# Performance work log

Measured on AMD Instinct MI355X. Metric: run time of the kernel, lower is better.

Reference implementation:

```python
import jax, jax.numpy as jnp
import numpy as np

NUM_HEADS = 8

def _mha(x, in_w, in_b, out_w, out_b):
    # x: [B, L, E]; in_w: [3E, E]; out_w: [E, E]
    B, L, E = x.shape
    H = NUM_HEADS
    Dh = E // H
    qkv = x @ in_w.T + in_b                      # [B, L, 3E]
    q, k, v = jnp.split(qkv, 3, axis=-1)
    # [B, H, L, Dh]
    q = q.reshape(B, L, H, Dh).transpose(0, 2, 1, 3)
    k = k.reshape(B, L, H, Dh).transpose(0, 2, 1, 3)
    v = v.reshape(B, L, H, Dh).transpose(0, 2, 1, 3)
    scale = 1.0 / jnp.sqrt(jnp.asarray(Dh, dtype=x.dtype))
    scores = jnp.einsum('bhld,bhsd->bhls', q, k) * scale   # [B, H, L, S]
    attn = jax.nn.softmax(scores, axis=-1)
    ctx = jnp.einsum('bhls,bhsd->bhld', attn, v)           # [B, H, L, Dh]
    ctx = ctx.transpose(0, 2, 1, 3).reshape(B, L, E)
    out = ctx @ out_w.T + out_b                             # [B, L, E]
    # PyTorch default average_attn_weights=True: mean over heads -> [B, L, S]
    weights = attn.mean(axis=1)
    return out, weights

def setup_inputs() -> dict:
    key = jax.random.key(0)
    ks = jax.random.split(key, 5)
    B, L, E = 4, 2048, 1024
    s = 0.02
    return {
        'hidden_states': jax.random.normal(ks[0], (B, L, E), dtype=jnp.float32),
        'in_proj_w': jax.random.normal(ks[1], (3 * E, E), dtype=jnp.float32) * s,
        'in_proj_b': jnp.zeros((3 * E,), dtype=jnp.float32),
        'out_proj_w': jax.random.normal(ks[2], (E, E), dtype=jnp.float32) * s,
        'out_proj_b': jnp.zeros((E,), dtype=jnp.float32),
        'dep_proj_w': jax.random.normal(ks[3], (E, E), dtype=jnp.float32) * s,
        'dep_proj_b': jnp.zeros((E,), dtype=jnp.float32),
    }

def reference(hidden_states, in_proj_w, in_proj_b, out_proj_w, out_proj_b, dep_proj_w, dep_proj_b):
    enhanced, attn_weights = _mha(hidden_states, in_proj_w, in_proj_b, out_proj_w, out_proj_b)
    # dependency_scores: mean over query dim then key dim -> [B]
    dependency_scores = attn_weights.mean(axis=1).mean(axis=-1)
    enhanced = enhanced @ dep_proj_w.T + dep_proj_b
    return dependency_scores, enhanced
```

## Files before the change

kernel.cpp:

```cpp
#include <hip/hip_runtime.h>


typedef __attribute__((ext_vector_type(8))) short short8;
typedef __attribute__((ext_vector_type(4))) float float4v;
typedef __attribute__((ext_vector_type(4))) int int4v;
typedef __attribute__((ext_vector_type(2))) unsigned uint2v;

__device__ inline ushort f2bf(float f) {
  union { float f; unsigned u; } v; v.f = f;
  unsigned u = v.u;
  return (ushort)((u + 0x7FFFu + ((u >> 16) & 1u)) >> 16);
}
__device__ inline float bf2f(ushort h) {
  union { unsigned u; float f; } v; v.u = ((unsigned)h) << 16;
  return v.f;
}
__device__ inline unsigned cvtpk(float lo, float hi) {
  unsigned r;
  asm("v_cvt_pk_bf16_f32 %0, %1, %2" : "=v"(r) : "v"(lo), "v"(hi));
  return r;
}

__global__ __launch_bounds__(256)
void cvt_all(const float* __restrict__ X, const float* __restrict__ Wi,
             const float* __restrict__ Wd,
             ushort* __restrict__ Xb, ushort* __restrict__ Wib,
             ushort* __restrict__ Wdb) {
  size_t i = ((size_t)blockIdx.x * 256 + threadIdx.x) * 8;
  const float* src; ushort* dst;
  if (i < 8388608)        { src = X  + i;              dst = Xb  + i; }
  else if (i < 11534336)  { src = Wi + (i - 8388608);  dst = Wib + (i - 8388608); }
  else                    { src = Wd + (i - 11534336); dst = Wdb + (i - 11534336); }
  float4v a = *(const float4v*)(src);
  float4v b = *(const float4v*)(src + 4);
  ushort o[8];
  o[0] = f2bf(a.x); o[1] = f2bf(a.y); o[2] = f2bf(a.z); o[3] = f2bf(a.w);
  o[4] = f2bf(b.x); o[5] = f2bf(b.y); o[6] = f2bf(b.z); o[7] = f2bf(b.w);
  *(int4v*)dst = *(const int4v*)o;
}

__global__ __launch_bounds__(256)
void cvtT(const float* __restrict__ Wo, ushort* __restrict__ WoT) {
  __shared__ ushort Ts[64 * 72];
  const int t = threadIdx.x;
  const int ct = blockIdx.x * 64, rt = blockIdx.y * 64;
#pragma unroll
  for (int i = 0; i < 4; i++) {
    const int row = i * 16 + (t >> 4), col4 = (t & 15) * 4;
    float4v v = *(const float4v*)(Wo + (size_t)(rt + row) * 1024 + ct + col4);
    ushort o[4] = {f2bf(v.x), f2bf(v.y), f2bf(v.z), f2bf(v.w)};
    *(uint2v*)(Ts + row * 72 + col4) = *(const uint2v*)o;
  }
  __syncthreads();
#pragma unroll
  for (int it = 0; it < 2; it++) {
    const int c = it * 256 + t;
    const int oc = c >> 3, r8 = (c & 7) * 8;
    ushort o[8];
#pragma unroll
    for (int j = 0; j < 8; j++) o[j] = Ts[(r8 + j) * 72 + oc];
    *(int4v*)(WoT + (size_t)(ct + oc) * 1024 + rt + r8) = *(const int4v*)o;
  }
}

__global__ __launch_bounds__(64)
void bck(const float* __restrict__ Wd, const float* __restrict__ bo,
         const float* __restrict__ bd, float* __restrict__ bc,
         float* __restrict__ dep) {
  const int row = blockIdx.x, lane = threadIdx.x;
  float s = 0.f;
#pragma unroll
  for (int i = 0; i < 4; i++) {
    const int j = i * 256 + lane * 4;
    float4v w = *(const float4v*)(Wd + (size_t)row * 1024 + j);
    float4v b = *(const float4v*)(bo + j);
    s += w.x * b.x + w.y * b.y + w.z * b.z + w.w * b.w;
  }
#pragma unroll
  for (int off = 1; off <= 32; off <<= 1) s += __shfl_xor(s, off);
  if (lane == 0) bc[row] = s + bd[row];
  if (row < 4 && lane == 1) dep[row] = 1.0f / 2048.0f;
}

template <bool OUT_BF16>
__global__ __launch_bounds__(256, 2)
void gemm_bt(const ushort* __restrict__ A, const ushort* __restrict__ W,
             const float* __restrict__ bias, void* __restrict__ Cv,
             int M, int N, int K) {
  __shared__ ushort As[128 * 32];
  __shared__ ushort Bs[128 * 32];
  const int t = threadIdx.x;
  const int w = t >> 6;
  const int lane = t & 63;
  const int m16 = lane & 15, quad = lane >> 4;
  const int bx = blockIdx.x, by = blockIdx.y;
  const int warpRow = w >> 1, warpCol = w & 1;

  const int srow = t >> 2;
  const int scol = (t & 3) * 8;
  const ushort* Aptr = A + (size_t)(by * 128) * K;
  const ushort* Wptr = W + (size_t)(bx * 128) * K;

  float4v zero4 = {0.f, 0.f, 0.f, 0.f};
  float4v acc[4][4];
#pragma unroll
  for (int i = 0; i < 4; i++)
#pragma unroll
    for (int j = 0; j < 4; j++) acc[i][j] = zero4;

  for (int k0 = 0; k0 < K; k0 += 32) {
    __syncthreads();
#pragma unroll
    for (int r = 0; r < 2; r++) {
      const ushort* g = Aptr + (size_t)(r * 64 + srow) * K + (k0 + scol);
      __builtin_amdgcn_global_load_lds(
          (const __attribute__((address_space(1))) void*)g,
          (__attribute__((address_space(3))) void*)(As + r * 2048 + t * 8),
          16, 0, 0);
    }
#pragma unroll
    for (int r = 0; r < 2; r++) {
      const ushort* g = Wptr + (size_t)(r * 64 + srow) * K + (k0 + scol);
      __builtin_amdgcn_global_load_lds(
          (const __attribute__((address_space(1))) void*)g,
          (__attribute__((address_space(3))) void*)(Bs + r * 2048 + t * 8),
          16, 0, 0);
    }
    __syncthreads();

    short8 af[4], bf[4];
#pragma unroll
    for (int i = 0; i < 4; i++) {
      af[i] = *(const short8*)(As + (warpRow * 64 + i * 16 + m16) * 32 + quad * 8);
      bf[i] = *(const short8*)(Bs + (warpCol * 64 + i * 16 + m16) * 32 + quad * 8);
    }
#pragma unroll
    for (int i = 0; i < 4; i++)
#pragma unroll
      for (int j = 0; j < 4; j++)
        acc[i][j] = __builtin_amdgcn_mfma_f32_16x16x32_bf16(af[i], bf[j],
                                                            acc[i][j], 0, 0, 0);
  }

  const int crow_base = by * 128 + warpRow * 64;
  const int ccol_base = bx * 128 + warpCol * 64;
#pragma unroll
  for (int j = 0; j < 4; j++) {
    const int col = ccol_base + j * 16 + m16;
    const float bv = bias ? bias[col] : 0.0f;
#pragma unroll
    for (int i = 0; i < 4; i++) {
      const int row = crow_base + i * 16 + quad * 4;
#pragma unroll
      for (int r = 0; r < 4; r++) {
        const float v = acc[i][j][r] + bv;
        if constexpr (OUT_BF16)
          ((ushort*)Cv)[(size_t)(row + r) * N + col] = f2bf(v);
        else
          ((float*)Cv)[(size_t)(row + r) * N + col] = v;
      }
    }
  }
}

__global__ __launch_bounds__(256, 2)
void gemm_qkv(const ushort* __restrict__ Xb, const ushort* __restrict__ Wib,
              const float* __restrict__ bi, ushort* __restrict__ qkv,
              ushort* __restrict__ Vt,
              const ushort* __restrict__ A2, const ushort* __restrict__ W2,
              ushort* __restrict__ C2) {
  __shared__ ushort As[128 * 32];
  __shared__ ushort Bs[128 * 32];
  const int t = threadIdx.x;
  const int w = t >> 6;
  const int lane = t & 63;
  const int m16 = lane & 15, quad = lane >> 4;
  const int bid = blockIdx.x;
  const bool second = bid >= 1536;
  int bx, by;
  const ushort *A, *W;
  if (!second) { bx = bid % 24; by = bid / 24; A = Xb; W = Wib; }
  else { const int b2 = bid - 1536; bx = b2 & 7; by = b2 >> 3; A = A2; W = W2; }
  const int warpRow = w >> 1, warpCol = w & 1;
  const int K = 1024;

  const int srow = t >> 2;
  const int scol = (t & 3) * 8;
  const ushort* Aptr = A + (size_t)(by * 128) * K;
  const ushort* Wptr = W + (size_t)(bx * 128) * K;

  float4v zero4 = {0.f, 0.f, 0.f, 0.f};
  float4v acc[4][4];
#pragma unroll
  for (int i = 0; i < 4; i++)
#pragma unroll
    for (int j = 0; j < 4; j++) acc[i][j] = zero4;

  for (int k0 = 0; k0 < K; k0 += 32) {
    __syncthreads();
#pragma unroll
    for (int r = 0; r < 2; r++) {
      const ushort* g = Aptr + (size_t)(r * 64 + srow) * K + (k0 + scol);
      __builtin_amdgcn_global_load_lds(
          (const __attribute__((address_space(1))) void*)g,
          (__attribute__((address_space(3))) void*)(As + r * 2048 + t * 8),
          16, 0, 0);
    }
#pragma unroll
    for (int r = 0; r < 2; r++) {
      const ushort* g = Wptr + (size_t)(r * 64 + srow) * K + (k0 + scol);
      __builtin_amdgcn_global_load_lds(
          (const __attribute__((address_space(1))) void*)g,
          (__attribute__((address_space(3))) void*)(Bs + r * 2048 + t * 8),
          16, 0, 0);
    }
    __syncthreads();

    short8 af[4], bf[4];
#pragma unroll
    for (int i = 0; i < 4; i++) {
      af[i] = *(const short8*)(As + (warpRow * 64 + i * 16 + m16) * 32 + quad * 8);
      bf[i] = *(const short8*)(Bs + (warpCol * 64 + i * 16 + m16) * 32 + quad * 8);
    }
#pragma unroll
    for (int i = 0; i < 4; i++)
#pragma unroll
      for (int j = 0; j < 4; j++)
        acc[i][j] = __builtin_amdgcn_mfma_f32_16x16x32_bf16(af[i], bf[j],
                                                            acc[i][j], 0, 0, 0);
  }

  const int crow_base = by * 128 + warpRow * 64;
  const int ccol_base = bx * 128 + warpCol * 64;

  if (second) {
#pragma unroll
    for (int j = 0; j < 4; j++) {
      const int col = ccol_base + j * 16 + m16;
#pragma unroll
      for (int i = 0; i < 4; i++) {
        const int row = crow_base + i * 16 + quad * 4;
#pragma unroll
        for (int r = 0; r < 4; r++)
          C2[(size_t)(row + r) * 1024 + col] = f2bf(acc[i][j][r]);
      }
    }
  } else if (bx < 16) {
#pragma unroll
    for (int j = 0; j < 4; j++) {
      const int col = ccol_base + j * 16 + m16;
      const float bv = bi[col];
#pragma unroll
      for (int i = 0; i < 4; i++) {
        const int row = crow_base + i * 16 + quad * 4;
#pragma unroll
        for (int r = 0; r < 4; r++)
          qkv[(size_t)(row + r) * 3072 + col] = f2bf(acc[i][j][r] + bv);
      }
    }
  } else {
    const int b = by >> 4;
#pragma unroll
    for (int j = 0; j < 4; j++) {
      const int col = ccol_base + j * 16 + m16;
      const float bv = bi[col];
      const int vcol = col - 2048;
      const int h = vcol >> 7, d = vcol & 127;
      ushort* vrow = Vt + (size_t)((b * 8 + h) * 128 + d) * 2048;
#pragma unroll
      for (int i = 0; i < 4; i++) {
        const int pos = ((by & 15) << 7) + warpRow * 64 + ((i >> 1) << 5) +
                        (2 * quad + (i & 1)) * 4;
        uint2v o;
        o.x = cvtpk(acc[i][j][0] + bv, acc[i][j][1] + bv);
        o.y = cvtpk(acc[i][j][2] + bv, acc[i][j][3] + bv);
        *(uint2v*)(vrow + pos) = o;
      }
    }
  }
}

__global__ __launch_bounds__(256, 2)
void attn(const ushort* __restrict__ qkv, const ushort* __restrict__ Vt,
          ushort* __restrict__ ctx) {
  __shared__ ushort Ks[2][64 * 128];
  __shared__ ushort Vsm[2][128 * 64];
  const int t = threadIdx.x, w = t >> 6, lane = t & 63;
  const int m16 = lane & 15, quad = lane >> 4;
  const int qt = blockIdx.x, h = blockIdx.y, b = blockIdx.z;
  const int E3 = 3072;
  const size_t bbase = (size_t)b * 2048;

  const ushort* Qg = qkv + (bbase + qt * 128 + w * 32) * E3 + h * 128;
  const ushort* Kg = qkv + bbase * E3 + 1024 + h * 128;
  const ushort* Vg = Vt + (size_t)((b * 8 + h) * 128) * 2048;

  auto stage = [&](int kt, int buf) {
#pragma unroll
    for (int it = 0; it < 4; it++) {
      const int c = it * 256 + t;
      const int row = c >> 4, cir = c & 15;
      const int j = (cir & 8) | ((cir ^ row) & 7);
      const ushort* g = Kg + (size_t)(kt * 64 + row) * E3 + j * 8;
      __builtin_amdgcn_global_load_lds(
          (const __attribute__((address_space(1))) void*)g,
          (__attribute__((address_space(3))) void*)(&Ks[buf][c * 8]), 16, 0, 0);
    }
#pragma unroll
    for (int it = 0; it < 4; it++) {
      const int c = it * 256 + t;
      const int d = c >> 3, cir = c & 7;
      const int j = cir ^ (d & 7);
      const ushort* g = Vg + (size_t)d * 2048 + kt * 64 + j * 8;
      __builtin_amdgcn_global_load_lds(
          (const __attribute__((address_space(1))) void*)g,
          (__attribute__((address_space(3))) void*)(&Vsm[buf][c * 8]), 16, 0, 0);
    }
  };

  stage(0, 0);

  const float c1 = 0.08838834764831845f * 1.4426950408889634f;
  short8 qf[2][4];
#pragma unroll
  for (int g = 0; g < 2; g++)
#pragma unroll
    for (int ks = 0; ks < 4; ks++) {
      short8 raw = *(const short8*)(Qg + (size_t)(g * 16 + m16) * E3 + ks * 32 + quad * 8);
      short8 s;
#pragma unroll
      for (int j = 0; j < 8; j++) s[j] = (short)f2bf(bf2f((ushort)raw[j]) * c1);
      qf[g][ks] = s;
    }

  int kslot[4];
#pragma unroll
  for (int ks = 0; ks < 4; ks++) {
    const int j = ks * 4 + quad;
    kslot[ks] = (j & 8) | ((j ^ m16) & 7);
  }

  float4v zero4 = {0.f, 0.f, 0.f, 0.f};
  float4v Oacc[2][8];
#pragma unroll
  for (int g = 0; g < 2; g++)
#pragma unroll
    for (int dt = 0; dt < 8; dt++) Oacc[g][dt] = zero4;
  float lsum[2] = {0.f, 0.f};

  for (int kt = 0; kt < 32; kt++) {
    const int cur = kt & 1;
    __syncthreads();
    if (kt < 31) stage(kt + 1, cur ^ 1);
    const ushort* Ksb = Ks[cur];
    const ushort* Vsb = Vsm[cur];

#pragma unroll
    for (int half = 0; half < 2; half++) {
      float4v st[2][2];
      st[0][0] = zero4; st[0][1] = zero4; st[1][0] = zero4; st[1][1] = zero4;
      __builtin_amdgcn_s_setprio(1);
#pragma unroll
      for (int ks = 0; ks < 4; ks++) {
#pragma unroll
        for (int mt2 = 0; mt2 < 2; mt2++) {
          short8 kf = *(const short8*)(Ksb + ((half * 2 + mt2) * 16 + m16) * 128 +
                                       kslot[ks] * 8);
          st[0][mt2] = __builtin_amdgcn_mfma_f32_16x16x32_bf16(kf, qf[0][ks], st[0][mt2], 0, 0, 0);
          st[1][mt2] = __builtin_amdgcn_mfma_f32_16x16x32_bf16(kf, qf[1][ks], st[1][mt2], 0, 0, 0);
        }
      }
      __builtin_amdgcn_s_setprio(0);
      short8 pfr[2];
#pragma unroll
      for (int g = 0; g < 2; g++) {
        unsigned pk[4];
#pragma unroll
        for (int mt2 = 0; mt2 < 2; mt2++) {
          float p0 = __builtin_exp2f(st[g][mt2][0]);
          float p1 = __builtin_exp2f(st[g][mt2][1]);
          float p2 = __builtin_exp2f(st[g][mt2][2]);
          float p3 = __builtin_exp2f(st[g][mt2][3]);
          lsum[g] += (p0 + p1) + (p2 + p3);
          pk[mt2 * 2]     = cvtpk(p0, p1);
          pk[mt2 * 2 + 1] = cvtpk(p2, p3);
        }
        union { int4v i; short8 s; } pf;
        pf.i.x = (int)pk[0];
        pf.i.y = (int)pk[1];
        pf.i.z = (int)pk[2];
        pf.i.w = (int)pk[3];
        pfr[g] = pf.s;
      }
      __builtin_amdgcn_s_setprio(1);
#pragma unroll
      for (int dt = 0; dt < 8; dt++) {
        const int vslot = (half * 4 + quad) ^ (m16 & 7);
        short8 vf = *(const short8*)(Vsb + (dt * 16 + m16) * 64 + vslot * 8);
        Oacc[0][dt] = __builtin_amdgcn_mfma_f32_16x16x32_bf16(pfr[0], vf, Oacc[0][dt], 0, 0, 0);
        Oacc[1][dt] = __builtin_amdgcn_mfma_f32_16x16x32_bf16(pfr[1], vf, Oacc[1][dt], 0, 0, 0);
      }
      __builtin_amdgcn_s_setprio(0);
    }
  }

#pragma unroll
  for (int g = 0; g < 2; g++) {
    float l = lsum[g];
    l += __shfl_xor(l, 16);
    l += __shfl_xor(l, 32);
    float* lf = (float*)(&Ks[0][w * 64]);
    lf[m16] = l;
    float linv[4];
#pragma unroll
    for (int r = 0; r < 4; r++) linv[r] = 1.0f / lf[quad * 4 + r];
#pragma unroll
    for (int r = 0; r < 4; r++) {
      const int row = qt * 128 + w * 32 + g * 16 + quad * 4 + r;
      ushort* crow = ctx + (bbase + row) * 1024 + h * 128;
#pragma unroll
      for (int dt = 0; dt < 8; dt++)
        crow[dt * 16 + m16] = f2bf(Oacc[g][dt][r] * linv[r]);
    }
  }
}

extern "C" void kernel_launch(void* const* d_in, const int* in_sizes, int n_in,
                              void* d_out, int out_size, void* d_ws, size_t ws_size,
                              hipStream_t stream) {
  const float* X  = (const float*)d_in[0];
  const float* Wi = (const float*)d_in[1];
  const float* bi = (const float*)d_in[2];
  const float* Wo = (const float*)d_in[3];
  const float* bo = (const float*)d_in[4];
  const float* Wd = (const float*)d_in[5];
  const float* bd = (const float*)d_in[6];
  float* out = (float*)d_out;

  ushort* p    = (ushort*)d_ws;
  ushort* Xb   = p; p += (size_t)8192 * 1024;
  ushort* Wib  = p; p += (size_t)3072 * 1024;
  ushort* WoTb = p; p += (size_t)1024 * 1024;
  ushort* Wdb  = p; p += (size_t)1024 * 1024;
  ushort* qkv  = p; p += (size_t)8192 * 3072;
  ushort* Vt   = p; p += (size_t)4096 * 2048;
  float*  bc   = (float*)p; p += 2048;
  ushort* WcbSep = p; p += (size_t)1024 * 1024;
  const size_t need_merged = (size_t)((char*)p - (char*)d_ws);
  const bool merged = ws_size >= need_merged;

  ushort* ctx = Xb;
  ushort* Wcb = merged ? WcbSep : Wib;

  cvt_all<<<6144, 256, 0, stream>>>(X, Wi, Wd, Xb, Wib, Wdb);
  cvtT<<<dim3(16, 16), 256, 0, stream>>>(Wo, WoTb);
  bck<<<1024, 64, 0, stream>>>(Wd, bo, bd, bc, out);
  if (merged) {
    gemm_qkv<<<1600, 256, 0, stream>>>(Xb, Wib, bi, qkv, Vt, Wdb, WoTb, Wcb);
  } else {
    gemm_qkv<<<1536, 256, 0, stream>>>(Xb, Wib, bi, qkv, Vt, Wdb, WoTb, nullptr);
    gemm_bt<true><<<dim3(8, 8), 256, 0, stream>>>(Wdb, WoTb, nullptr, Wcb,
                                                  1024, 1024, 1024);
  }
  attn<<<dim3(16, 8, 4), 256, 0, stream>>>(qkv, Vt, ctx);
  gemm_bt<false><<<dim3(8, 64), 256, 0, stream>>>(ctx, Wcb, bc, out + 4, 8192, 1024, 1024);
}
```

Before: 300.2 us.

## Fuse weight prep, combined-weight GEMM and bias fold into one prep kernel

Merges the conversion kernels, the Wo transpose, the bias-fold kernel and the Wd·Wo combined-weight GEMM into a single prep launch. The combined weight is now computed directly from fp32 inputs with a small 64x64 MFMA tile, and the QKV GEMM no longer carries extra blocks for it. The attention inner loop also issues both halves' QK MFMAs before the exp/PV phase, to give more independent MFMA work. This cuts launches and intermediate bf16 weight buffers, but the in-prep GEMM runs on only 256 small blocks with scalar transposed LDS stores, which may lengthen the critical path.

Measured after the change: 309.8 us. 1.03x slower.

```diff
diff --git a/kernel.cpp b/kernel.cpp
--- a/kernel.cpp
+++ b/kernel.cpp
@@ -22,64 +22,100 @@
 }
 
 __global__ __launch_bounds__(256)
-void cvt_all(const float* __restrict__ X, const float* __restrict__ Wi,
-             const float* __restrict__ Wd,
-             ushort* __restrict__ Xb, ushort* __restrict__ Wib,
-             ushort* __restrict__ Wdb) {
-  size_t i = ((size_t)blockIdx.x * 256 + threadIdx.x) * 8;
-  const float* src; ushort* dst;
-  if (i < 8388608)        { src = X  + i;              dst = Xb  + i; }
-  else if (i < 11534336)  { src = Wi + (i - 8388608);  dst = Wib + (i - 8388608); }
-  else                    { src = Wd + (i - 11534336); dst = Wdb + (i - 11534336); }
-  float4v a = *(const float4v*)(src);
-  float4v b = *(const float4v*)(src + 4);
-  ushort o[8];
-  o[0] = f2bf(a.x); o[1] = f2bf(a.y); o[2] = f2bf(a.z); o[3] = f2bf(a.w);
-  o[4] = f2bf(b.x); o[5] = f2bf(b.y); o[6] = f2bf(b.z); o[7] = f2bf(b.w);
-  *(int4v*)dst = *(const int4v*)o;
-}
-
-__global__ __launch_bounds__(256)
-void cvtT(const float* __restrict__ Wo, ushort* __restrict__ WoT) {
-  __shared__ ushort Ts[64 * 72];
+void prep(const float* __restrict__ X, const float* __restrict__ Wi,
+          const float* __restrict__ Wd, const float* __restrict__ Wo,
+          const float* __restrict__ bo, const float* __restrict__ bd,
+          ushort* __restrict__ Xb, ushort* __restrict__ Wib,
+          ushort* __restrict__ Wcb, float* __restrict__ bc,
+          float* __restrict__ dep) {
+  __shared__ ushort As[64 * 32];
+  __shared__ ushort Bs[64 * 40];
+  const int bid = blockIdx.x;
   const int t = threadIdx.x;
-  const int ct = blockIdx.x * 64, rt = blockIdx.y * 64;
-#pragma unroll
-  for (int i = 0; i < 4; i++) {
-    const int row = i * 16 + (t >> 4), col4 = (t & 15) * 4;
-    float4v v = *(const float4v*)(Wo + (size_t)(rt + row) * 1024 + ct + col4);
-    ushort o[4] = {f2bf(v.x), f2bf(v.y), f2bf(v.z), f2bf(v.w)};
-    *(uint2v*)(Ts + row * 72 + col4) = *(const uint2v*)o;
-  }
-  __syncthreads();
-#pragma unroll
-  for (int it = 0; it < 2; it++) {
-    const int c = it * 256 + t;
-    const int oc = c >> 3, r8 = (c & 7) * 8;
+
+  if (bid < 256) {
+    const int bx = bid & 15, by = bid >> 4;
+    const int w = t >> 6, lane = t & 63;
+    const int m16 = lane & 15, quad = lane >> 4;
+    const int warpRow = w >> 1, warpCol = w & 1;
+    float4v zero4 = {0.f, 0.f, 0.f, 0.f};
+    float4v acc[2][2];
+    acc[0][0] = zero4; acc[0][1] = zero4; acc[1][0] = zero4; acc[1][1] = zero4;
+
+    const int an = t >> 2, ar8 = (t & 3) * 8;
+    const int br = t >> 3, bk8 = (t & 7) * 8;
+
+    for (int r0 = 0; r0 < 1024; r0 += 32) {
+      {
+        const float* g = Wd + (size_t)(by * 64 + an) * 1024 + r0 + ar8;
+        float4v a0 = *(const float4v*)g;
+        float4v a1 = *(const float4v*)(g + 4);
+        ushort o[8] = {f2bf(a0.x), f2bf(a0.y), f2bf(a0.z), f2bf(a0.w),
+                       f2bf(a1.x), f2bf(a1.y), f2bf(a1.z), f2bf(a1.w)};
+        *(int4v*)(As + an * 32 + ar8) = *(const int4v*)o;
+      }
+      {
+        const float* g = Wo + (size_t)(r0 + br) * 1024 + bx * 64 + bk8;
+        float4v b0 = *(const float4v*)g;
+        float4v b1 = *(const float4v*)(g + 4);
+        ushort o[8] = {f2bf(b0.x), f2bf(b0.y), f2bf(b0.z), f2bf(b0.w),
+                       f2bf(b1.x), f2bf(b1.y), f2bf(b1.z), f2bf(b1.w)};
+#pragma unroll
+        for (int j = 0; j < 8; j++) Bs[(bk8 + j) * 40 + br] = o[j];
+      }
+      __syncthreads();
+      short8 af[2], bf[2];
+#pragma unroll
+      for (int i = 0; i < 2; i++) {
+        af[i] = *(const short8*)(As + (warpRow * 32 + i * 16 + m16) * 32 + quad * 8);
+        bf[i] = *(const short8*)(Bs + (warpCol * 32 + i * 16 + m16) * 40 + quad * 8);
+      }
+#pragma unroll
+      for (int i = 0; i < 2; i++)
+#pragma unroll
+        for (int j = 0; j < 2; j++)
+          acc[i][j] = __builtin_amdgcn_mfma_f32_16x16x32_bf16(af[i], bf[j],
+                                                              acc[i][j], 0, 0, 0);
+      __syncthreads();
+    }
+#pragma unroll
+    for (int j = 0; j < 2; j++) {
+      const int col = bx * 64 + warpCol * 32 + j * 16 + m16;
+#pragma unroll
+      for (int i = 0; i < 2; i++) {
+        const int row = by * 64 + warpRow * 32 + i * 16 + quad * 4;
+#pragma unroll
+        for (int r = 0; r < 4; r++)
+          Wcb[(size_t)(row + r) * 1024 + col] = f2bf(acc[i][j][r]);
+      }
+    }
+  } else if (bid < 512) {
+    const int w = t >> 6, lane = t & 63;
+    const int row = (bid - 256) * 4 + w;
+    float s = 0.f;
+#pragma unroll
+    for (int i = 0; i < 4; i++) {
+      const int j = i * 256 + lane * 4;
+      float4v wv = *(const float4v*)(Wd + (size_t)row * 1024 + j);
+      float4v bv = *(const float4v*)(bo + j);
+      s += wv.x * bv.x + wv.y * bv.y + wv.z * bv.z + wv.w * bv.w;
+    }
+#pragma unroll
+    for (int off = 1; off <= 32; off <<= 1) s += __shfl_xor(s, off);
+    if (lane == 0) bc[row] = s + bd[row];
+    if (row < 4 && lane == 1) dep[row] = 1.0f / 2048.0f;
+  } else {
+    size_t i = ((size_t)(bid - 512) * 256 + t) * 8;
+    const float* src; ushort* dst;
+    if (i < 8388608) { src = X + i;             dst = Xb + i; }
+    else             { src = Wi + (i - 8388608); dst = Wib + (i - 8388608); }
+    float4v a = *(const float4v*)(src);
+    float4v b = *(const float4v*)(src + 4);
     ushort o[8];
-#pragma unroll
-    for (int j = 0; j < 8; j++) o[j] = Ts[(r8 + j) * 72 + oc];
-    *(int4v*)(WoT + (size_t)(ct + oc) * 1024 + rt + r8) = *(const int4v*)o;
-  }
-}
-
-__global__ __launch_bounds__(64)
-void bck(const float* __restrict__ Wd, const float* __restrict__ bo,
-         const float* __restrict__ bd, float* __restrict__ bc,
-         float* __restrict__ dep) {
-  const int row = blockIdx.x, lane = threadIdx.x;
-  float s = 0.f;
-#pragma unroll
-  for (int i = 0; i < 4; i++) {
-    const int j = i * 256 + lane * 4;
-    float4v w = *(const float4v*)(Wd + (size_t)row * 1024 + j);
-    float4v b = *(const float4v*)(bo + j);
-    s += w.x * b.x + w.y * b.y + w.z * b.z + w.w * b.w;
-  }
-#pragma unroll
-  for (int off = 1; off <= 32; off <<= 1) s += __shfl_xor(s, off);
-  if (lane == 0) bc[row] = s + bd[row];
-  if (row < 4 && lane == 1) dep[row] = 1.0f / 2048.0f;
+    o[0] = f2bf(a.x); o[1] = f2bf(a.y); o[2] = f2bf(a.z); o[3] = f2bf(a.w);
+    o[4] = f2bf(b.x); o[5] = f2bf(b.y); o[6] = f2bf(b.z); o[7] = f2bf(b.w);
+    *(int4v*)dst = *(const int4v*)o;
+  }
 }
 
 template <bool OUT_BF16>
@@ -166,28 +202,21 @@
 __global__ __launch_bounds__(256, 2)
 void gemm_qkv(const ushort* __restrict__ Xb, const ushort* __restrict__ Wib,
               const float* __restrict__ bi, ushort* __restrict__ qkv,
-              ushort* __restrict__ Vt,
-              const ushort* __restrict__ A2, const ushort* __restrict__ W2,
-              ushort* __restrict__ C2) {
+              ushort* __restrict__ Vt) {
   __shared__ ushort As[128 * 32];
   __shared__ ushort Bs[128 * 32];
   const int t = threadIdx.x;
   const int w = t >> 6;
   const int lane = t & 63;
   const int m16 = lane & 15, quad = lane >> 4;
-  const int bid = blockIdx.x;
-  const bool second = bid >= 1536;
-  int bx, by;
-  const ushort *A, *W;
-  if (!second) { bx = bid % 24; by = bid / 24; A = Xb; W = Wib; }
-  else { const int b2 = bid - 1536; bx = b2 & 7; by = b2 >> 3; A = A2; W = W2; }
+  const int bx = blockIdx.x, by = blockIdx.y;
   const int warpRow = w >> 1, warpCol = w & 1;
   const int K = 1024;
 
   const int srow = t >> 2;
   const int scol = (t & 3) * 8;
-  const ushort* Aptr = A + (size_t)(by * 128) * K;
-  const ushort* Wptr = W + (size_t)(bx * 128) * K;
+  const ushort* Aptr = Xb + (size_t)(by * 128) * K;
+  const ushort* Wptr = Wib + (size_t)(bx * 128) * K;
 
   float4v zero4 = {0.f, 0.f, 0.f, 0.f};
   float4v acc[4][4];
@@ -233,19 +262,7 @@
   const int crow_base = by * 128 + warpRow * 64;
   const int ccol_base = bx * 128 + warpCol * 64;
 
-  if (second) {
-#pragma unroll
-    for (int j = 0; j < 4; j++) {
-      const int col = ccol_base + j * 16 + m16;
-#pragma unroll
-      for (int i = 0; i < 4; i++) {
-        const int row = crow_base + i * 16 + quad * 4;
-#pragma unroll
-        for (int r = 0; r < 4; r++)
-          C2[(size_t)(row + r) * 1024 + col] = f2bf(acc[i][j][r]);
-      }
-    }
-  } else if (bx < 16) {
+  if (bx < 16) {
 #pragma unroll
     for (int j = 0; j < 4; j++) {
       const int col = ccol_base + j * 16 + m16;
@@ -339,6 +356,8 @@
     const int j = ks * 4 + quad;
     kslot[ks] = (j & 8) | ((j ^ m16) & 7);
   }
+  const int vslot0 = (0 * 4 + quad) ^ (m16 & 7);
+  const int vslot1 = (1 * 4 + quad) ^ (m16 & 7);
 
   float4v zero4 = {0.f, 0.f, 0.f, 0.f};
   float4v Oacc[2][8];
@@ -355,32 +374,40 @@
     const ushort* Ksb = Ks[cur];
     const ushort* Vsb = Vsm[cur];
 
+    float4v st[2][2][2];
 #pragma unroll
     for (int half = 0; half < 2; half++) {
-      float4v st[2][2];
-      st[0][0] = zero4; st[0][1] = zero4; st[1][0] = zero4; st[1][1] = zero4;
-      __builtin_amdgcn_s_setprio(1);
-#pragma unroll
-      for (int ks = 0; ks < 4; ks++) {
+      st[half][0][0] = zero4; st[half][0][1] = zero4;
+      st[half][1][0] = zero4; st[half][1][1] = zero4;
+    }
+    __builtin_amdgcn_s_setprio(1);
+#pragma unroll
+    for (int half = 0; half < 2; half++)
+#pragma unroll
+      for (int ks = 0; ks < 4; ks++)
 #pragma unroll
         for (int mt2 = 0; mt2 < 2; mt2++) {
           short8 kf = *(const short8*)(Ksb + ((half * 2 + mt2) * 16 + m16) * 128 +
                                        kslot[ks] * 8);
-          st[0][mt2] = __builtin_amdgcn_mfma_f32_16x16x32_bf16(kf, qf[0][ks], st[0][mt2], 0, 0, 0);
-          st[1][mt2] = __builtin_amdgcn_mfma_f32_16x16x32_bf16(kf, qf[1][ks], st[1][mt2], 0, 0, 0);
+          st[half][0][mt2] = __builtin_amdgcn_mfma_f32_16x16x32_bf16(
+              kf, qf[0][ks], st[half][0][mt2], 0, 0, 0);
+          st[half][1][mt2] = __builtin_amdgcn_mfma_f32_16x16x32_bf16(
+              kf, qf[1][ks], st[half][1][mt2], 0, 0, 0);
         }
-      }
-      __builtin_amdgcn_s_setprio(0);
+    __builtin_amdgcn_s_setprio(0);
+
+#pragma unroll
+    for (int half = 0; half < 2; half++) {
       short8 pfr[2];
 #pragma unroll
       for (int g = 0; g < 2; g++) {
         unsigned pk[4];
 #pragma unroll
         for (int mt2 = 0; mt2 < 2; mt2++) {
-          float p0 = __builtin_exp2f(st[g][mt2][0]);
-          float p1 = __builtin_exp2f(st[g][mt2][1]);
-          float p2 = __builtin_exp2f(st[g][mt2][2]);
-          float p3 = __builtin_exp2f(st[g][mt2][3]);
+          float p0 = __builtin_exp2f(st[half][g][mt2][0]);
+          float p1 = __builtin_exp2f(st[half][g][mt2][1]);
+          float p2 = __builtin_exp2f(st[half][g][mt2][2]);
+          float p3 = __builtin_exp2f(st[half][g][mt2][3]);
           lsum[g] += (p0 + p1) + (p2 + p3);
           pk[mt2 * 2]     = cvtpk(p0, p1);
           pk[mt2 * 2 + 1] = cvtpk(p2, p3);
@@ -392,10 +419,10 @@
         pf.i.w = (int)pk[3];
         pfr[g] = pf.s;
       }
+      const int vslot = half ? vslot1 : vslot0;
       __builtin_amdgcn_s_setprio(1);
 #pragma unroll
       for (int dt = 0; dt < 8; dt++) {
-        const int vslot = (half * 4 + quad) ^ (m16 & 7);
         short8 vf = *(const short8*)(Vsb + (dt * 16 + m16) * 64 + vslot * 8);
         Oacc[0][dt] = __builtin_amdgcn_mfma_f32_16x16x32_bf16(pfr[0], vf, Oacc[0][dt], 0, 0, 0);
         Oacc[1][dt] = __builtin_amdgcn_mfma_f32_16x16x32_bf16(pfr[1], vf, Oacc[1][dt], 0, 0, 0);
@@ -440,28 +467,16 @@
   ushort* p    = (ushort*)d_ws;
   ushort* Xb   = p; p += (size_t)8192 * 1024;
   ushort* Wib  = p; p += (size_t)3072 * 1024;
-  ushort* WoTb = p; p += (size_t)1024 * 1024;
-  ushort* Wdb  = p; p += (size_t)1024 * 1024;
+  ushort* Wcb  = p; p += (size_t)1024 * 1024;
+  p += (size_t)1024 * 1024;
   ushort* qkv  = p; p += (size_t)8192 * 3072;
   ushort* Vt   = p; p += (size_t)4096 * 2048;
-  float*  bc   = (float*)p; p += 2048;
-  ushort* WcbSep = p; p += (size_t)1024 * 1024;
-  const size_t need_merged = (size_t)((char*)p - (char*)d_ws);
-  const bool merged = ws_size >= need_merged;
-
-  ushort* ctx = Xb;
-  ushort* Wcb = merged ? WcbSep : Wib;
-
-  cvt_all<<<6144, 256, 0, stream>>>(X, Wi, Wd, Xb, Wib, Wdb);
-  cvtT<<<dim3(16, 16), 256, 0, stream>>>(Wo, WoTb);
-  bck<<<1024, 64, 0, stream>>>(Wd, bo, bd, bc, out);
-  if (merged) {
-    gemm_qkv<<<1600, 256, 0, stream>>>(Xb, Wib, bi, qkv, Vt, Wdb, WoTb, Wcb);
-  } else {
-    gemm_qkv<<<1536, 256, 0, stream>>>(Xb, Wib, bi, qkv, Vt, Wdb, WoTb, nullptr);
-    gemm_bt<true><<<dim3(8, 8), 256, 0, stream>>>(Wdb, WoTb, nullptr, Wcb,
-                                                  1024, 1024, 1024);
-  }
+  float*  bc   = (float*)p;
+  ushort* ctx  = Xb;
+
+  prep<<<6144, 256, 0, stream>>>(X, Wi, Wd, Wo, bo, bd, Xb, Wib, Wcb, bc, out);
+  gemm_qkv<<<dim3(24, 64), 256, 0, stream>>>(Xb, Wib, bi, qkv, Vt);
   attn<<<dim3(16, 8, 4), 256, 0, stream>>>(qkv, Vt, ctx);
-  gemm_bt<false><<<dim3(8, 64), 256, 0, stream>>>(ctx, Wcb, bc, out + 4, 8192, 1024, 1024);
-}
+  gemm_bt<false><<<dim3(8, 64), 256, 0, stream>>>(ctx, Wcb, bc, out + 4,
+                                                  8192, 1024, 1024);
+}
```
